# Kernel optimization log

Hardware: AMD Instinct MI355X
Metric: run time of the kernel (lower is better)

The kernel has to match this reference:

```python
import jax, jax.numpy as jnp
import numpy as np
from jax import lax

F = 64          # nb_filters
K_DOWN = 4      # size_kernel_sample
K_RES = 3       # size_kernel_res
DIL = 3         # rate_dilation_res
N_DOWN = 3      # downsampling blocks (one level)
N_RES = 4       # residual sub-blocks per block
N_EMB = 512     # codebook size
BETA = 0.25


def conv1d(x, w, b, stride=1, dil=1, act=True):
    # x: (B,T,C), w: (K,Cin,Cout)
    y = lax.conv_general_dilated(x, w, (stride,), 'SAME', rhs_dilation=(dil,),
                                 dimension_numbers=('NWC', 'WIO', 'NWC')) + b
    return jax.nn.relu(y) if act else y


def conv1d_t(x, w, b, stride):
    # transposed conv, w: (K, Cin, Cout)
    y = lax.conv_transpose(x, w, (stride,), 'SAME',
                           dimension_numbers=('NWC', 'WIO', 'NWC')) + b
    return jax.nn.relu(y)


def setup_inputs() -> dict:
    key = jax.random.key(0)
    ks = jax.random.split(key, 12)
    s_in = 1.0 / np.sqrt(K_DOWN * 1)
    s_f = 1.0 / np.sqrt(K_DOWN * F)
    s_r = 1.0 / np.sqrt(K_RES * F)
    return {
        'x': jax.random.normal(ks[0], (4, 65536, 1), dtype=jnp.float32),
        'w_down0': jax.random.normal(ks[1], (K_DOWN, 1, F), dtype=jnp.float32) * s_in,
        'b_down0': jnp.zeros((F,), jnp.float32),
        'w_down': jax.random.normal(ks[2], (N_DOWN - 1, K_DOWN, F, F), dtype=jnp.float32) * s_f,
        'b_down': jnp.zeros((N_DOWN - 1, F), jnp.float32),
        'w_res_enc': jax.random.normal(ks[3], (N_DOWN, N_RES, 2, K_RES, F, F), dtype=jnp.float32) * s_r,
        'b_res_enc': jnp.zeros((N_DOWN, N_RES, 2, F), jnp.float32),
        'codebook': jax.random.normal(ks[4], (N_EMB, F), dtype=jnp.float32),
        'w_res_dec': jax.random.normal(ks[5], (N_DOWN, N_RES, 2, K_RES, F, F), dtype=jnp.float32) * s_r,
        'b_res_dec': jnp.zeros((N_DOWN, N_RES, 2, F), jnp.float32),
        'w_up': jax.random.normal(ks[6], (N_DOWN, K_DOWN, F, F), dtype=jnp.float32) * s_f,
        'b_up': jnp.zeros((N_DOWN, F), jnp.float32),
        'w_proj': jax.random.normal(ks[7], (K_RES, F, 1), dtype=jnp.float32) * s_r,
        'b_proj': jnp.zeros((1,), jnp.float32),
    }


def reference(x, w_down0, b_down0, w_down, b_down, w_res_enc, b_res_enc,
              codebook, w_res_dec, b_res_dec, w_up, b_up, w_proj, b_proj):
    # ---- Encoder: N_DOWN stride-2 downsampling blocks, each followed by
    # N_RES ForwardResidualSubBlocks (dilated conv -> conv, residual add) ----
    h = conv1d(x, w_down0, b_down0, stride=2)
    for blk in range(N_DOWN):
        if blk > 0:
            h = conv1d(h, w_down[blk - 1], b_down[blk - 1], stride=2)
        for r in range(N_RES):
            y = conv1d(h, w_res_enc[blk, r, 0], b_res_enc[blk, r, 0], dil=DIL)
            y = conv1d(y, w_res_enc[blk, r, 1], b_res_enc[blk, r, 1], dil=1)
            h = h + y
    z_e = h  # (B, T/8, F)

    # ---- VectorQuantiser over channel axis ----
    dot = jnp.einsum('btd,kd->btk', z_e, codebook)          # tensordot
    nz = jnp.sum(jnp.square(z_e), axis=-1, keepdims=True)   # (B,T,1)
    ne = jnp.sum(jnp.square(codebook), axis=-1)             # (K,)
    dist = -2.0 * dot + nz + ne                             # squared cdist
    ids = jnp.argmin(dist, axis=-1)                         # (B,T)
    z_q = codebook[ids]                                     # embedding_lookup
    loss_commit = jnp.mean(jnp.linalg.norm(lax.stop_gradient(z_e) - z_q, axis=-1))
    loss_codebook = jnp.mean(jnp.linalg.norm(z_e - lax.stop_gradient(z_q), axis=-1))
    loss_vq = loss_codebook + BETA * loss_commit
    similarity = dot / jnp.sqrt(nz) / jnp.sqrt(ne)

    # ---- Decoder: residual blocks then stride-2 transposed conv, x N_DOWN ----
    h = z_q
    for blk in range(N_DOWN):
        for r in range(N_RES):
            y = conv1d(h, w_res_dec[blk, r, 0], b_res_dec[blk, r, 0], dil=1)
            y = conv1d(y, w_res_dec[blk, r, 1], b_res_dec[blk, r, 1], dil=DIL)
            h = h + y
        h = conv1d_t(h, w_up[blk], b_up[blk], stride=2)
    x_hat = conv1d(h, w_proj, b_proj, act=False)  # linear projection
    return x_hat, loss_vq, ids, similarity
```

## Files before the change

kernel.cpp:

```cpp
#include <hip/hip_runtime.h>
#include <cstdint>


#define OFF_LOSS 262144
#define OFF_IDS  262145
#define OFF_SIM  294913

__global__ __launch_bounds__(256) void down0_kernel(
    const float* __restrict__ x, const float* __restrict__ w,
    const float* __restrict__ bias, float* __restrict__ y)
{
  int idx = blockIdx.x * 256 + threadIdx.x;
  int co = idx & 63;
  int r  = idx >> 6;
  int t  = r & 32767;
  int b  = r >> 15;
  const float* xb = x + (size_t)b * 65536;
  float acc = bias[co];
  #pragma unroll
  for (int k = 0; k < 4; ++k) {
    int gt = 2 * t - 1 + k;
    float xv = ((unsigned)gt < 65536u) ? xb[gt] : 0.f;
    acc += xv * w[k * 64 + co];
  }
  y[(size_t)idx] = fmaxf(acc, 0.f);
}

template <int DIL, bool HAS_RES>
__global__ __launch_bounds__(512, 8) void conv3_kernel(
    const float* __restrict__ x, const float* __restrict__ w,
    const float* __restrict__ bias, const float* res,
    float* y, int T)
{
  constexpr int TT = 128;
  constexpr int XT = TT + 2 * DIL;
  constexpr int XS = XT + 1;
  __shared__ float xs[64 * XS];
  const int tid  = threadIdx.x;
  const int lane = tid & 63;
  const int b    = blockIdx.y;
  const int t0   = blockIdx.x * TT;
  const int wv   = __builtin_amdgcn_readfirstlane(tid >> 6);
  const int co0  = __builtin_amdgcn_readfirstlane(wv * 8);

  const float* xb = x + (size_t)b * T * 64;
  for (int e = tid; e < 16 * XT; e += 512) {
    int tl = e >> 4, cq = (e & 15) * 4;
    int gt = t0 - DIL + tl;
    float4 v = make_float4(0.f, 0.f, 0.f, 0.f);
    if ((unsigned)gt < (unsigned)T) v = *(const float4*)&xb[(size_t)gt * 64 + cq];
    xs[(cq + 0) * XS + tl] = v.x;
    xs[(cq + 1) * XS + tl] = v.y;
    xs[(cq + 2) * XS + tl] = v.z;
    xs[(cq + 3) * XS + tl] = v.w;
  }
  __syncthreads();

  float acc0[8] = {}, acc1[8] = {};
  const float* wb = w + co0;
  for (int ci = 0; ci < 64; ++ci) {
    const float* xr = xs + ci * XS + lane;
    float a0 = xr[0],  a1 = xr[DIL],      a2 = xr[2 * DIL];
    float b0 = xr[64], b1 = xr[64 + DIL], b2 = xr[64 + 2 * DIL];
    const float* w0 = wb + (0 * 64 + ci) * 64;
    const float* w1 = wb + (1 * 64 + ci) * 64;
    const float* w2 = wb + (2 * 64 + ci) * 64;
    #pragma unroll
    for (int j = 0; j < 8; ++j) {
      float c0 = w0[j], c1 = w1[j], c2 = w2[j];
      acc0[j] = fmaf(a0, c0, fmaf(a1, c1, fmaf(a2, c2, acc0[j])));
      acc1[j] = fmaf(b0, c0, fmaf(b1, c1, fmaf(b2, c2, acc1[j])));
    }
  }

  size_t o0 = ((size_t)b * T + t0 + lane) * 64 + co0;
  size_t o1 = o0 + (size_t)64 * 64;
  float r0[8], r1[8];
  #pragma unroll
  for (int j = 0; j < 8; ++j) {
    float bj = bias[co0 + j];
    r0[j] = fmaxf(acc0[j] + bj, 0.f);
    r1[j] = fmaxf(acc1[j] + bj, 0.f);
  }
  if (HAS_RES) {
    #pragma unroll
    for (int q = 0; q < 2; ++q) {
      float4 v0 = *(const float4*)&res[o0 + 4 * q];
      float4 v1 = *(const float4*)&res[o1 + 4 * q];
      r0[4*q+0] += v0.x; r0[4*q+1] += v0.y; r0[4*q+2] += v0.z; r0[4*q+3] += v0.w;
      r1[4*q+0] += v1.x; r1[4*q+1] += v1.y; r1[4*q+2] += v1.z; r1[4*q+3] += v1.w;
    }
  }
  #pragma unroll
  for (int q = 0; q < 2; ++q) {
    *(float4*)&y[o0 + 4 * q] = make_float4(r0[4*q], r0[4*q+1], r0[4*q+2], r0[4*q+3]);
    *(float4*)&y[o1 + 4 * q] = make_float4(r1[4*q], r1[4*q+1], r1[4*q+2], r1[4*q+3]);
  }
}

__global__ __launch_bounds__(512, 8) void down2_kernel(
    const float* __restrict__ x, const float* __restrict__ w,
    const float* __restrict__ bias, float* __restrict__ y, int Tin)
{
  constexpr int XT = 130, XS = 131;
  __shared__ float xs[64 * XS];
  const int tid  = threadIdx.x;
  const int lane = tid & 63;
  const int b    = blockIdx.y;
  const int t0   = blockIdx.x * 64;
  const int Tout = Tin >> 1;
  const int wv   = __builtin_amdgcn_readfirstlane(tid >> 6);
  const int co0  = __builtin_amdgcn_readfirstlane(wv * 8);

  const float* xb = x + (size_t)b * Tin * 64;
  for (int e = tid; e < 16 * XT; e += 512) {
    int tl = e >> 4, cq = (e & 15) * 4;
    int gt = 2 * t0 - 1 + tl;
    float4 v = make_float4(0.f, 0.f, 0.f, 0.f);
    if ((unsigned)gt < (unsigned)Tin) v = *(const float4*)&xb[(size_t)gt * 64 + cq];
    xs[(cq + 0) * XS + tl] = v.x;
    xs[(cq + 1) * XS + tl] = v.y;
    xs[(cq + 2) * XS + tl] = v.z;
    xs[(cq + 3) * XS + tl] = v.w;
  }
  __syncthreads();

  float acc[8] = {};
  const float* wb = w + co0;
  for (int ci = 0; ci < 64; ++ci) {
    const float* xr = xs + ci * XS + 2 * lane;
    float a0 = xr[0], a1 = xr[1], a2 = xr[2], a3 = xr[3];
    const float* w0 = wb + (0 * 64 + ci) * 64;
    const float* w1 = wb + (1 * 64 + ci) * 64;
    const float* w2 = wb + (2 * 64 + ci) * 64;
    const float* w3 = wb + (3 * 64 + ci) * 64;
    #pragma unroll
    for (int j = 0; j < 8; ++j)
      acc[j] = fmaf(a0, w0[j], fmaf(a1, w1[j], fmaf(a2, w2[j], fmaf(a3, w3[j], acc[j]))));
  }

  size_t o = ((size_t)b * Tout + t0 + lane) * 64 + co0;
  #pragma unroll
  for (int q = 0; q < 2; ++q) {
    float4 rr;
    rr.x = fmaxf(acc[4*q+0] + bias[co0 + 4*q+0], 0.f);
    rr.y = fmaxf(acc[4*q+1] + bias[co0 + 4*q+1], 0.f);
    rr.z = fmaxf(acc[4*q+2] + bias[co0 + 4*q+2], 0.f);
    rr.w = fmaxf(acc[4*q+3] + bias[co0 + 4*q+3], 0.f);
    *(float4*)&y[o + 4 * q] = rr;
  }
}

__global__ __launch_bounds__(512, 8) void up_kernel(
    const float* __restrict__ x, const float* __restrict__ w,
    const float* __restrict__ bias, float* __restrict__ y, int Tin)
{
  constexpr int XT = 66, XS = 67;
  __shared__ float xs[64 * XS];
  const int tid  = threadIdx.x;
  const int lane = tid & 63;
  const int b    = blockIdx.y;
  const int u0   = blockIdx.x * 64;
  const int Tout = Tin << 1;
  const int wv   = __builtin_amdgcn_readfirstlane(tid >> 6);
  const int co0  = __builtin_amdgcn_readfirstlane(wv * 8);

  const float* xb = x + (size_t)b * Tin * 64;
  for (int e = tid; e < 16 * XT; e += 512) {
    int ul = e >> 4, cq = (e & 15) * 4;
    int gu = u0 - 1 + ul;
    float4 v = make_float4(0.f, 0.f, 0.f, 0.f);
    if ((unsigned)gu < (unsigned)Tin) v = *(const float4*)&xb[(size_t)gu * 64 + cq];
    xs[(cq + 0) * XS + ul] = v.x;
    xs[(cq + 1) * XS + ul] = v.y;
    xs[(cq + 2) * XS + ul] = v.z;
    xs[(cq + 3) * XS + ul] = v.w;
  }
  __syncthreads();

  float acce[8] = {}, acco[8] = {};
  const float* wb = w + co0;
  for (int ci = 0; ci < 64; ++ci) {
    const float* xr = xs + ci * XS + lane;
    float a0 = xr[0], a1 = xr[1], a2 = xr[2];
    const float* w0 = wb + (0 * 64 + ci) * 64;
    const float* w1 = wb + (1 * 64 + ci) * 64;
    const float* w2 = wb + (2 * 64 + ci) * 64;
    const float* w3 = wb + (3 * 64 + ci) * 64;
    #pragma unroll
    for (int j = 0; j < 8; ++j) {
      acce[j] = fmaf(a0, w0[j], fmaf(a1, w2[j], acce[j]));
      acco[j] = fmaf(a1, w1[j], fmaf(a2, w3[j], acco[j]));
    }
  }

  size_t oe = ((size_t)b * Tout + 2 * (u0 + lane)) * 64 + co0;
  size_t oo = oe + 64;
  #pragma unroll
  for (int q = 0; q < 2; ++q) {
    float4 re, ro;
    re.x = fmaxf(acce[4*q+0] + bias[co0 + 4*q+0], 0.f);
    re.y = fmaxf(acce[4*q+1] + bias[co0 + 4*q+1], 0.f);
    re.z = fmaxf(acce[4*q+2] + bias[co0 + 4*q+2], 0.f);
    re.w = fmaxf(acce[4*q+3] + bias[co0 + 4*q+3], 0.f);
    ro.x = fmaxf(acco[4*q+0] + bias[co0 + 4*q+0], 0.f);
    ro.y = fmaxf(acco[4*q+1] + bias[co0 + 4*q+1], 0.f);
    ro.z = fmaxf(acco[4*q+2] + bias[co0 + 4*q+2], 0.f);
    ro.w = fmaxf(acco[4*q+3] + bias[co0 + 4*q+3], 0.f);
    *(float4*)&y[oe + 4 * q] = re;
    *(float4*)&y[oo + 4 * q] = ro;
  }
}

__global__ __launch_bounds__(256) void proj_kernel(
    const float* __restrict__ x, const float* __restrict__ w,
    const float* __restrict__ bias, float* __restrict__ out)
{
  const int lane = threadIdx.x & 63;
  const int wid  = (blockIdx.x * 256 + threadIdx.x) >> 6;
  const float w0 = w[lane], w1 = w[64 + lane], w2 = w[128 + lane];
  const float bb = bias[0];
  size_t base = (size_t)wid * 64;
  for (int i = 0; i < 64; ++i) {
    size_t tau = base + i;
    int b = (int)(tau >> 16);
    int t = (int)(tau & 65535);
    const float* xb = x + ((size_t)b * 65536) * 64;
    float pm = (t > 0)     ? xb[(size_t)(t - 1) * 64 + lane] : 0.f;
    float pc =               xb[(size_t)t * 64 + lane];
    float pp = (t < 65535) ? xb[(size_t)(t + 1) * 64 + lane] : 0.f;
    float s = pm * w0 + pc * w1 + pp * w2;
    #pragma unroll
    for (int off = 32; off; off >>= 1) s += __shfl_down(s, off);
    if (lane == 0) out[tau] = s + bb;
  }
}

__global__ __launch_bounds__(256) void nz_kernel(
    const float* __restrict__ ze, float* __restrict__ nz)
{
  int lane = threadIdx.x & 63;
  int tok  = (blockIdx.x * 256 + threadIdx.x) >> 6;
  float v = ze[(size_t)tok * 64 + lane];
  float s = v * v;
  #pragma unroll
  for (int off = 32; off; off >>= 1) s += __shfl_down(s, off);
  if (lane == 0) nz[tok] = s;
}

#define VQA_TOKS 32
__global__ __launch_bounds__(256) void vq_dots_kernel(
    const float* __restrict__ ze, const float* __restrict__ cb,
    const float* __restrict__ nzbuf, float* __restrict__ sim_out,
    float2* __restrict__ pmin)
{
  const int tid = threadIdx.x;
  const int c = blockIdx.y * 256 + tid;
  float r[64];
  #pragma unroll
  for (int q = 0; q < 16; ++q) {
    float4 a = ((const float4*)cb)[(size_t)c * 16 + q];
    r[4*q] = a.x; r[4*q+1] = a.y; r[4*q+2] = a.z; r[4*q+3] = a.w;
  }
  float ne = 0.f;
  #pragma unroll
  for (int d = 0; d < 64; ++d) ne += r[d] * r[d];
  const float rsne = 1.f / sqrtf(ne);
  const int wvid = tid >> 6;

  for (int it = 0; it < VQA_TOKS; ++it) {
    const int tok = blockIdx.x * VQA_TOKS + it;
    const float* zt = ze + (size_t)tok * 64;
    float d0 = 0.f, d1 = 0.f;
    #pragma unroll
    for (int d = 0; d < 64; d += 8) {
      d0 = fmaf(zt[d+0], r[d+0], fmaf(zt[d+1], r[d+1], fmaf(zt[d+2], r[d+2], fmaf(zt[d+3], r[d+3], d0))));
      d1 = fmaf(zt[d+4], r[d+4], fmaf(zt[d+5], r[d+5], fmaf(zt[d+6], r[d+6], fmaf(zt[d+7], r[d+7], d1))));
    }
    float dot = d0 + d1;
    const float nzv = nzbuf[tok];
    float dist = (-2.f * dot + nzv) + ne;
    sim_out[(size_t)tok * 512 + c] = dot * (1.f / sqrtf(nzv)) * rsne;

    float md = dist; int mi = c;
    #pragma unroll
    for (int off = 32; off; off >>= 1) {
      float od = __shfl_down(md, off);
      int   oi = __shfl_down(mi, off);
      if (od < md || (od == md && oi < mi)) { md = od; mi = oi; }
    }
    if ((tid & 63) == 0) pmin[tok * 8 + blockIdx.y * 4 + wvid] = make_float2(md, (float)mi);
  }
}

__global__ __launch_bounds__(256) void vq_finish_kernel(
    const float* __restrict__ ze, const float* __restrict__ cb,
    const float2* __restrict__ pmin, float* __restrict__ zq,
    float* __restrict__ ids_out, float* __restrict__ blocksum)
{
  const int tid = threadIdx.x;
  const int lane = tid & 63, wvid = tid >> 6;
  float lloss = 0.f;
  for (int it = 0; it < 16; ++it) {
    const int tok = blockIdx.x * 64 + wvid * 16 + it;
    float bd = 1e30f; int bi = 0;
    #pragma unroll
    for (int p = 0; p < 8; ++p) {
      float2 pr = pmin[tok * 8 + p];
      float d = pr.x; int i = (int)pr.y;
      if (d < bd || (d == bd && i < bi)) { bd = d; bi = i; }
    }
    float zev = ze[(size_t)tok * 64 + lane];
    float cv  = cb[(size_t)bi * 64 + lane];
    float df = zev - cv;
    float s = df * df;
    #pragma unroll
    for (int off = 32; off; off >>= 1) s += __shfl_down(s, off);
    zq[(size_t)tok * 64 + lane] = cv;
    if (lane == 0) { ids_out[tok] = (float)bi; lloss += sqrtf(s); }
  }
  __shared__ float ls[4];
  if (lane == 0) ls[wvid] = lloss;
  __syncthreads();
  if (tid == 0) blocksum[blockIdx.x] = ls[0] + ls[1] + ls[2] + ls[3];
}

__global__ void loss_fin_kernel(const float* __restrict__ blocksum,
                                float* __restrict__ out)
{
  const int lane = threadIdx.x;
  float s = 0.f;
  for (int i = lane; i < 512; i += 64) s += blocksum[i];
  #pragma unroll
  for (int off = 32; off; off >>= 1) s += __shfl_down(s, off);
  if (lane == 0) out[0] = 1.25f * s / 32768.f;
}

extern "C" void kernel_launch(void* const* d_in, const int* in_sizes, int n_in,
                              void* d_out, int out_size, void* d_ws, size_t ws_size,
                              hipStream_t stream)
{
  const float* x       = (const float*)d_in[0];
  const float* w_down0 = (const float*)d_in[1];
  const float* b_down0 = (const float*)d_in[2];
  const float* w_down  = (const float*)d_in[3];
  const float* b_down  = (const float*)d_in[4];
  const float* w_res_e = (const float*)d_in[5];
  const float* b_res_e = (const float*)d_in[6];
  const float* cb      = (const float*)d_in[7];
  const float* w_res_d = (const float*)d_in[8];
  const float* b_res_d = (const float*)d_in[9];
  const float* w_up    = (const float*)d_in[10];
  const float* b_up    = (const float*)d_in[11];
  const float* w_proj  = (const float*)d_in[12];
  const float* b_proj  = (const float*)d_in[13];

  float* out = (float*)d_out;
  const size_t BUF = (size_t)4 * 65536 * 64;
  float*  bufA     = (float*)d_ws;
  float*  bufB     = bufA + BUF;
  float*  nzbuf    = bufB + BUF;
  float2* pmin     = (float2*)(nzbuf + 32768);
  float*  blocksum = (float*)(pmin + 32768 * 8);

  float* h = bufA;
  float* tmp = bufB;

  down0_kernel<<<32768, 256, 0, stream>>>(x, w_down0, b_down0, h);
  int T = 32768;
  for (int blk = 0; blk < 3; ++blk) {
    if (blk > 0) {
      down2_kernel<<<dim3(T / 2 / 64, 4), 512, 0, stream>>>(
          h, w_down + (size_t)(blk - 1) * 4 * 64 * 64, b_down + (blk - 1) * 64, tmp, T);
      T >>= 1;
      float* s = h; h = tmp; tmp = s;
    }
    for (int r = 0; r < 4; ++r) {
      const float* w0p = w_res_e + (((size_t)blk * 4 + r) * 2 + 0) * 3 * 64 * 64;
      const float* w1p = w_res_e + (((size_t)blk * 4 + r) * 2 + 1) * 3 * 64 * 64;
      const float* b0p = b_res_e + (((size_t)blk * 4 + r) * 2 + 0) * 64;
      const float* b1p = b_res_e + (((size_t)blk * 4 + r) * 2 + 1) * 64;
      conv3_kernel<3, false><<<dim3(T / 128, 4), 512, 0, stream>>>(h, w0p, b0p, nullptr, tmp, T);
      conv3_kernel<1, true ><<<dim3(T / 128, 4), 512, 0, stream>>>(tmp, w1p, b1p, h, h, T);
    }
  }

  nz_kernel<<<8192, 256, 0, stream>>>(h, nzbuf);
  vq_dots_kernel<<<dim3(32768 / VQA_TOKS, 2), 256, 0, stream>>>(h, cb, nzbuf, out + OFF_SIM, pmin);
  vq_finish_kernel<<<512, 256, 0, stream>>>(h, cb, pmin, tmp, out + OFF_IDS, blocksum);
  loss_fin_kernel<<<1, 64, 0, stream>>>(blocksum, out + OFF_LOSS);
  { float* s = h; h = tmp; tmp = s; }

  for (int blk = 0; blk < 3; ++blk) {
    for (int r = 0; r < 4; ++r) {
      const float* w0p = w_res_d + (((size_t)blk * 4 + r) * 2 + 0) * 3 * 64 * 64;
      const float* w1p = w_res_d + (((size_t)blk * 4 + r) * 2 + 1) * 3 * 64 * 64;
      const float* b0p = b_res_d + (((size_t)blk * 4 + r) * 2 + 0) * 64;
      const float* b1p = b_res_d + (((size_t)blk * 4 + r) * 2 + 1) * 64;
      conv3_kernel<1, false><<<dim3(T / 128, 4), 512, 0, stream>>>(h, w0p, b0p, nullptr, tmp, T);
      conv3_kernel<3, true ><<<dim3(T / 128, 4), 512, 0, stream>>>(tmp, w1p, b1p, h, h, T);
    }
    up_kernel<<<dim3(2 * T / 128, 4), 512, 0, stream>>>(
        h, w_up + (size_t)blk * 4 * 64 * 64, b_up + blk * 64, tmp, T);
    T <<= 1;
    float* s = h; h = tmp; tmp = s;
  }

  proj_kernel<<<1024, 256, 0, stream>>>(h, w_proj, b_proj, out);
}
```

Before: 1.787 ms.

## Register-block conv3 timesteps per lane, pick tile by T, stage VQ tokens in LDS

The residual conv kernel now gives each lane TPL consecutive timesteps and loads them from shared memory with float2 vector reads. It reuses the overlapping dilated taps in registers and pads the LDS row stride to a multiple of four. A smaller 64-timestep tile is used when T is below 16384, to keep more blocks in flight on the downsampled levels. The down and up kernels get padded strides and float2 LDS reads, and the VQ dot kernel stages its 32 token vectors in shared memory instead of reading them from global memory per codeword. Contiguous per-lane timesteps change the LDS and global store access patterns and may add bank conflicts or uncoalesced stores.

```diff
diff --git a/kernel.cpp b/kernel.cpp
--- a/kernel.cpp
+++ b/kernel.cpp
@@ -26,15 +26,17 @@
   y[(size_t)idx] = fmaxf(acc, 0.f);
 }
 
-template <int DIL, bool HAS_RES>
+template <int DIL, bool HAS_RES, int TT>
 __global__ __launch_bounds__(512, 8) void conv3_kernel(
     const float* __restrict__ x, const float* __restrict__ w,
     const float* __restrict__ bias, const float* res,
     float* y, int T)
 {
-  constexpr int TT = 128;
-  constexpr int XT = TT + 2 * DIL;
-  constexpr int XS = XT + 1;
+  constexpr int TPL = TT / 64;
+  constexpr int XT  = TT + 2 * DIL;
+  constexpr int XS0 = (XT + 3) & ~3;
+  constexpr int XS  = (XS0 % 8 == 4) ? XS0 : XS0 + 4;
+  constexpr int NV  = TPL + 2 * DIL;
   __shared__ float xs[64 * XS];
   const int tid  = threadIdx.x;
   const int lane = tid & 63;
@@ -56,45 +58,49 @@
   }
   __syncthreads();
 
-  float acc0[8] = {}, acc1[8] = {};
+  float acc[TPL][8] = {};
   const float* wb = w + co0;
+  const int tb = TPL * lane;
   for (int ci = 0; ci < 64; ++ci) {
-    const float* xr = xs + ci * XS + lane;
-    float a0 = xr[0],  a1 = xr[DIL],      a2 = xr[2 * DIL];
-    float b0 = xr[64], b1 = xr[64 + DIL], b2 = xr[64 + 2 * DIL];
+    const float* xr = xs + ci * XS + tb;
+    float xv[NV];
+    if constexpr (TPL == 2) {
+      const float2* p2 = (const float2*)xr;
+      #pragma unroll
+      for (int q = 0; q < NV / 2; ++q) { float2 v = p2[q]; xv[2*q] = v.x; xv[2*q+1] = v.y; }
+    } else {
+      #pragma unroll
+      for (int j = 0; j < NV; ++j) xv[j] = xr[j];
+    }
     const float* w0 = wb + (0 * 64 + ci) * 64;
     const float* w1 = wb + (1 * 64 + ci) * 64;
     const float* w2 = wb + (2 * 64 + ci) * 64;
     #pragma unroll
     for (int j = 0; j < 8; ++j) {
       float c0 = w0[j], c1 = w1[j], c2 = w2[j];
-      acc0[j] = fmaf(a0, c0, fmaf(a1, c1, fmaf(a2, c2, acc0[j])));
-      acc1[j] = fmaf(b0, c0, fmaf(b1, c1, fmaf(b2, c2, acc1[j])));
-    }
-  }
-
-  size_t o0 = ((size_t)b * T + t0 + lane) * 64 + co0;
-  size_t o1 = o0 + (size_t)64 * 64;
-  float r0[8], r1[8];
-  #pragma unroll
-  for (int j = 0; j < 8; ++j) {
-    float bj = bias[co0 + j];
-    r0[j] = fmaxf(acc0[j] + bj, 0.f);
-    r1[j] = fmaxf(acc1[j] + bj, 0.f);
-  }
-  if (HAS_RES) {
-    #pragma unroll
-    for (int q = 0; q < 2; ++q) {
-      float4 v0 = *(const float4*)&res[o0 + 4 * q];
-      float4 v1 = *(const float4*)&res[o1 + 4 * q];
-      r0[4*q+0] += v0.x; r0[4*q+1] += v0.y; r0[4*q+2] += v0.z; r0[4*q+3] += v0.w;
-      r1[4*q+0] += v1.x; r1[4*q+1] += v1.y; r1[4*q+2] += v1.z; r1[4*q+3] += v1.w;
-    }
-  }
-  #pragma unroll
-  for (int q = 0; q < 2; ++q) {
-    *(float4*)&y[o0 + 4 * q] = make_float4(r0[4*q], r0[4*q+1], r0[4*q+2], r0[4*q+3]);
-    *(float4*)&y[o1 + 4 * q] = make_float4(r1[4*q], r1[4*q+1], r1[4*q+2], r1[4*q+3]);
+      #pragma unroll
+      for (int i = 0; i < TPL; ++i)
+        acc[i][j] = fmaf(xv[i], c0, fmaf(xv[i + DIL], c1, fmaf(xv[i + 2 * DIL], c2, acc[i][j])));
+    }
+  }
+
+  float bs[8];
+  #pragma unroll
+  for (int j = 0; j < 8; ++j) bs[j] = bias[co0 + j];
+  #pragma unroll
+  for (int i = 0; i < TPL; ++i) {
+    size_t o = ((size_t)b * T + t0 + tb + i) * 64 + co0;
+    float r[8];
+    #pragma unroll
+    for (int j = 0; j < 8; ++j) r[j] = fmaxf(acc[i][j] + bs[j], 0.f);
+    if (HAS_RES) {
+      float4 v0 = *(const float4*)&res[o];
+      float4 v1 = *(const float4*)&res[o + 4];
+      r[0] += v0.x; r[1] += v0.y; r[2] += v0.z; r[3] += v0.w;
+      r[4] += v1.x; r[5] += v1.y; r[6] += v1.z; r[7] += v1.w;
+    }
+    *(float4*)&y[o]     = make_float4(r[0], r[1], r[2], r[3]);
+    *(float4*)&y[o + 4] = make_float4(r[4], r[5], r[6], r[7]);
   }
 }
 
@@ -102,7 +108,7 @@
     const float* __restrict__ x, const float* __restrict__ w,
     const float* __restrict__ bias, float* __restrict__ y, int Tin)
 {
-  constexpr int XT = 130, XS = 131;
+  constexpr int XT = 130, XS = 132;
   __shared__ float xs[64 * XS];
   const int tid  = threadIdx.x;
   const int lane = tid & 63;
@@ -128,8 +134,9 @@
   float acc[8] = {};
   const float* wb = w + co0;
   for (int ci = 0; ci < 64; ++ci) {
-    const float* xr = xs + ci * XS + 2 * lane;
-    float a0 = xr[0], a1 = xr[1], a2 = xr[2], a3 = xr[3];
+    const float2* p2 = (const float2*)(xs + ci * XS + 2 * lane);
+    float2 v0 = p2[0], v1 = p2[1];
+    float a0 = v0.x, a1 = v0.y, a2 = v1.x, a3 = v1.y;
     const float* w0 = wb + (0 * 64 + ci) * 64;
     const float* w1 = wb + (1 * 64 + ci) * 64;
     const float* w2 = wb + (2 * 64 + ci) * 64;
@@ -155,7 +162,7 @@
     const float* __restrict__ x, const float* __restrict__ w,
     const float* __restrict__ bias, float* __restrict__ y, int Tin)
 {
-  constexpr int XT = 66, XS = 67;
+  constexpr int XT = 66, XS = 68;
   __shared__ float xs[64 * XS];
   const int tid  = threadIdx.x;
   const int lane = tid & 63;
@@ -254,7 +261,14 @@
     const float* __restrict__ nzbuf, float* __restrict__ sim_out,
     float2* __restrict__ pmin)
 {
+  __shared__ float zs[VQA_TOKS * 64];
   const int tid = threadIdx.x;
+  {
+    const float4* src = (const float4*)(ze + (size_t)blockIdx.x * VQA_TOKS * 64);
+    float4* dst = (float4*)zs;
+    dst[tid]       = src[tid];
+    dst[tid + 256] = src[tid + 256];
+  }
   const int c = blockIdx.y * 256 + tid;
   float r[64];
   #pragma unroll
@@ -267,17 +281,17 @@
   for (int d = 0; d < 64; ++d) ne += r[d] * r[d];
   const float rsne = 1.f / sqrtf(ne);
   const int wvid = tid >> 6;
+  __syncthreads();
 
   for (int it = 0; it < VQA_TOKS; ++it) {
     const int tok = blockIdx.x * VQA_TOKS + it;
-    const float* zt = ze + (size_t)tok * 64;
-    float d0 = 0.f, d1 = 0.f;
-    #pragma unroll
-    for (int d = 0; d < 64; d += 8) {
-      d0 = fmaf(zt[d+0], r[d+0], fmaf(zt[d+1], r[d+1], fmaf(zt[d+2], r[d+2], fmaf(zt[d+3], r[d+3], d0))));
-      d1 = fmaf(zt[d+4], r[d+4], fmaf(zt[d+5], r[d+5], fmaf(zt[d+6], r[d+6], fmaf(zt[d+7], r[d+7], d1))));
-    }
-    float dot = d0 + d1;
+    const float4* z4 = (const float4*)(zs + it * 64);
+    float dot = 0.f;
+    #pragma unroll
+    for (int q = 0; q < 16; ++q) {
+      float4 zv = z4[q];
+      dot += zv.x * r[4*q] + zv.y * r[4*q+1] + zv.z * r[4*q+2] + zv.w * r[4*q+3];
+    }
     const float nzv = nzbuf[tok];
     float dist = (-2.f * dot + nzv) + ne;
     sim_out[(size_t)tok * 512 + c] = dot * (1.f / sqrtf(nzv)) * rsne;
@@ -335,6 +349,16 @@
   for (int off = 32; off; off >>= 1) s += __shfl_down(s, off);
   if (lane == 0) out[0] = 1.25f * s / 32768.f;
 }
+
+#define LAUNCH_CONV3(DILV, RESV, XP, WP, BP, RP, YP)                           \
+  do {                                                                         \
+    if (T >= 16384)                                                            \
+      conv3_kernel<DILV, RESV, 128><<<dim3(T / 128, 4), 512, 0, stream>>>(     \
+          XP, WP, BP, RP, YP, T);                                              \
+    else                                                                       \
+      conv3_kernel<DILV, RESV, 64><<<dim3(T / 64, 4), 512, 0, stream>>>(       \
+          XP, WP, BP, RP, YP, T);                                              \
+  } while (0)
 
 extern "C" void kernel_launch(void* const* d_in, const int* in_sizes, int n_in,
                               void* d_out, int out_size, void* d_ws, size_t ws_size,
@@ -380,8 +404,8 @@
       const float* w1p = w_res_e + (((size_t)blk * 4 + r) * 2 + 1) * 3 * 64 * 64;
       const float* b0p = b_res_e + (((size_t)blk * 4 + r) * 2 + 0) * 64;
       const float* b1p = b_res_e + (((size_t)blk * 4 + r) * 2 + 1) * 64;
-      conv3_kernel<3, false><<<dim3(T / 128, 4), 512, 0, stream>>>(h, w0p, b0p, nullptr, tmp, T);
-      conv3_kernel<1, true ><<<dim3(T / 128, 4), 512, 0, stream>>>(tmp, w1p, b1p, h, h, T);
+      LAUNCH_CONV3(3, false, h, w0p, b0p, nullptr, tmp);
+      LAUNCH_CONV3(1, true,  tmp, w1p, b1p, h, h);
     }
   }
 
@@ -397,8 +421,8 @@
       const float* w1p = w_res_d + (((size_t)blk * 4 + r) * 2 + 1) * 3 * 64 * 64;
       const float* b0p = b_res_d + (((size_t)blk * 4 + r) * 2 + 0) * 64;
       const float* b1p = b_res_d + (((size_t)blk * 4 + r) * 2 + 1) * 64;
-      conv3_kernel<1, false><<<dim3(T / 128, 4), 512, 0, stream>>>(h, w0p, b0p, nullptr, tmp, T);
-      conv3_kernel<3, true ><<<dim3(T / 128, 4), 512, 0, stream>>>(tmp, w1p, b1p, h, h, T);
+      LAUNCH_CONV3(1, false, h, w0p, b0p, nullptr, tmp);
+      LAUNCH_CONV3(3, true,  tmp, w1p, b1p, h, h);
     }
     up_kernel<<<dim3(2 * T / 128, 4), 512, 0, stream>>>(
         h, w_up + (size_t)blk * 4 * 64 * 64, b_up + blk * 64, tmp, T);
```

Result: faster. 1.691 ms (-5.4%).
